# Kernel optimization log

Measured on AMD Instinct MI355X. Metric: run time of the kernel, lower is better.

The kernel has to match this reference:

```python
import jax, jax.numpy as jnp
import numpy as np

B, S, E, H = 32, 4096, 256, 8
P, M = 256, 16  # positions per batch row, tokens per position (pileup depth)


def setup_inputs() -> dict:
    key = jax.random.key(0)
    k1, k2, k3, k4, k5, k6 = jax.random.split(key, 6)
    embeddings = jax.random.normal(k1, (B, S, E), jnp.float32)
    # each position 0..P-1 appears exactly M times per batch row, shuffled
    base = jnp.repeat(jnp.arange(P, dtype=jnp.int32), M)  # (S,)
    positions = jax.vmap(lambda k: jax.random.permutation(k, base))(jax.random.split(k2, B))
    scale = 1.0 / np.sqrt(E)
    Wq = jax.random.normal(k3, (E, E), jnp.float32) * scale
    Wk = jax.random.normal(k4, (E, E), jnp.float32) * scale
    Wv = jax.random.normal(k5, (E, E), jnp.float32) * scale
    W0 = jax.random.normal(k6, (E, E), jnp.float32) * scale
    return {"embeddings": embeddings, "Wq": Wq, "Wk": Wk, "Wv": Wv, "W0": W0,
            "positions": positions, "num_positions": P, "group_size": M, "num_heads": H}


def _intra_group_rank(positions):
    # rank[b,i] = number of earlier tokens j<i in row b with the same position
    Bb, Ss = positions.shape
    idx = jnp.arange(Ss)
    order = jnp.argsort(positions, axis=1)  # stable sort preserves original order within a group
    sp = jnp.take_along_axis(positions, order, axis=1)
    new_group = jnp.concatenate([jnp.ones((Bb, 1), bool), sp[:, 1:] != sp[:, :-1]], axis=1)
    group_start = jax.lax.cummax(jnp.where(new_group, idx[None, :], 0), axis=1)
    rank_sorted = idx[None, :] - group_start
    rank = jnp.zeros_like(positions).at[jnp.arange(Bb)[:, None], order].set(rank_sorted.astype(positions.dtype))
    return rank


def reference(embeddings, Wq, Wk, Wv, W0, positions, num_positions, group_size, num_heads):
    Bb, Ss, Ee = embeddings.shape
    Pp, Mm, Hh = num_positions, group_size, num_heads
    dh = Ee // Hh
    G = Bb * Pp

    valid = positions >= 0
    rank = _intra_group_rank(positions)                       # (B,S) slot within group
    gid = jnp.arange(Bb, dtype=positions.dtype)[:, None] * Pp + jnp.clip(positions, 0)  # (B,S)
    gid_scat = jnp.where(valid, gid, G)                        # out-of-bounds -> dropped

    # gather: ragged regroup into (G, M, E), zero-padded like the torch version
    grouped = jnp.zeros((G, Mm, Ee), embeddings.dtype).at[gid_scat, rank].set(embeddings, mode='drop')

    # multi-head self-attention within each group (no mask, matching the original)
    q = (grouped @ Wq).reshape(G, Mm, Hh, dh)
    k = (grouped @ Wk).reshape(G, Mm, Hh, dh)
    v = (grouped @ Wv).reshape(G, Mm, Hh, dh)
    scores = jnp.einsum('gmhd,gnhd->ghmn', q, k) / np.sqrt(dh).astype(embeddings.dtype)
    attn = jax.nn.softmax(scores, axis=-1)
    ctx = jnp.einsum('ghmn,gnhd->gmhd', attn, v).reshape(G, Mm, Ee)
    att_out = ctx @ W0                                         # (G, M, E)

    # scatter back; invalid (-1) slots stay zero, as in the torch loop
    out = jnp.where(valid[:, :, None], att_out[gid, rank], 0.0)
    return out
```

## Files before the change

kernel.cpp:

```cpp
#include <hip/hip_runtime.h>
#include <stdint.h>

#define B_    32
#define S_    4096
#define E_    256
#define P_    256
#define M_    16
#define G_    (B_*P_)
#define NSLOT (G_*M_)
#define GPW   8
#define ROWS  128
#define NWG   (G_/GPW)

typedef float fv4 __attribute__((ext_vector_type(4)));
typedef int   iv4 __attribute__((ext_vector_type(4)));
typedef int   iv2 __attribute__((ext_vector_type(2)));
typedef __bf16 bv8 __attribute__((ext_vector_type(8)));
typedef short  sv4 __attribute__((ext_vector_type(4)));

__device__ __forceinline__ uint32_t bf16rne(float f) {
  uint32_t u = __builtin_bit_cast(uint32_t, f);
  u += 0x7fffu + ((u >> 16) & 1u);
  return u >> 16;
}
__device__ __forceinline__ uint32_t pk2(uint32_t lo, uint32_t hi) {
  return (lo & 0xffffu) | (hi << 16);
}
__device__ __forceinline__ void mfma32(fv4& d, iv4 a, iv4 b) {
  d = __builtin_amdgcn_mfma_f32_16x16x32_bf16(
        __builtin_bit_cast(bv8, a), __builtin_bit_cast(bv8, b), d, 0, 0, 0);
}
__device__ __forceinline__ void mfma16(fv4& d, iv2 a, iv2 b) {
  d = __builtin_amdgcn_mfma_f32_16x16x16bf16_1k(
        __builtin_bit_cast(sv4, a), __builtin_bit_cast(sv4, b), d, 0, 0, 0);
}
__device__ __forceinline__ void gload_lds16(const void* g, void* l) {
  __builtin_amdgcn_global_load_lds(
      (const __attribute__((address_space(1))) uint32_t*)g,
      (__attribute__((address_space(3))) uint32_t*)l, 16, 0, 0);
}

#define SWZ(off, row) ((off) ^ (((row) & 7) << 4))
#define LQKV(row, cb) ( ((row) >> 1) * 128 + \
    (((((row) & 1) << 6) + (cb)) ^ ((((row) >> 1) & 7) << 4)) )

#define BAR()   { asm volatile("" ::: "memory"); __builtin_amdgcn_s_barrier(); \
                  asm volatile("" ::: "memory"); }
#define VMWAIT1 asm volatile("s_waitcnt vmcnt(1)" ::: "memory")
#define VMWAIT0 asm volatile("s_waitcnt vmcnt(0)" ::: "memory")
#define LGKM0   asm volatile("s_waitcnt lgkmcnt(0)" ::: "memory")

__global__ void k_init(int* cnt, int* s2t) {
  int i = blockIdx.x * 256 + threadIdx.x;
  if (i < G_) cnt[i] = 0;
  if (i < NSLOT) s2t[i] = -1;
}

__global__ void k_trans(const float* __restrict__ Wq, const float* __restrict__ Wk,
                        const float* __restrict__ Wv, const float* __restrict__ W0,
                        uint16_t* __restrict__ WT) {
  int o = blockIdx.x * 256 + threadIdx.x;
  int wsel = blockIdx.y;
  const float* W = (wsel == 0) ? Wq : (wsel == 1) ? Wk : (wsel == 2) ? Wv : W0;
  int n = o >> 8, k = o & 255;
  WT[(size_t)wsel * 65536 + o] = (uint16_t)bf16rne(W[k * 256 + n]);
}

__global__ void k_rank(const int* __restrict__ pos, int* cnt, int* s2t) {
  int i = blockIdx.x * 256 + threadIdx.x;
  if (i >= B_ * S_) return;
  int p = pos[i];
  if (p < 0 || p >= P_) return;
  int b = i >> 12;
  int g = (b << 8) + p;
  int r = atomicAdd(&cnt[g], 1);
  if (r < M_) s2t[g * M_ + r] = i;
}

__device__ __forceinline__ void stage_qkv(const uint16_t* Wt, int c0, char* buf,
                                          int w, int l) {
  int n = w * 2 + (l >> 5);
  int seg = l & 31;
  gload_lds16(reinterpret_cast<const char*>(Wt) + (size_t)(c0 + n) * 512 + SWZ(seg * 16, n),
              buf + w * 1024);
}
__device__ __forceinline__ void stage_w0(const uint16_t* W0T, int c0, char* buf,
                                         int w, int l) {
  int pair = w * 8 + (l >> 3);
  int jp = ((l & 7) * 16) ^ ((pair & 7) << 4);
  int n = 2 * pair + (jp >> 6);
  gload_lds16(reinterpret_cast<const char*>(W0T) + (size_t)n * 512 + c0 * 2 + (jp & 63),
              buf + w * 1024);
}

__global__ __launch_bounds__(1024, 1) void k_main(
    const float* __restrict__ emb, const int* __restrict__ s2t,
    const uint16_t* __restrict__ WT, float* __restrict__ out) {
  extern __shared__ char smem[];
  char* bufA = smem;
  char* bufB = smem + 16384;
  char* Qb = smem + 32768;
  char* Kb = smem + 40960;
  char* Vb = smem + 49152;
  char* Cb = smem + 57344;

  const uint16_t* WqT = WT;
  const uint16_t* WkT = WT + 65536;
  const uint16_t* WvT = WT + 131072;
  const uint16_t* W0T = WT + 196608;

  const int tid = threadIdx.x;
  const int l = tid & 63;
  const int w = tid >> 6;
  const int lane15 = l & 15;
  const int lq = l >> 4;
  const int rb = w >> 1;
  const int ch = w & 1;
  const int slot0 = blockIdx.x * ROWS;

  #pragma unroll 2
  for (int rl = 0; rl < 8; ++rl) {
    int row = w * 8 + rl;
    int t = s2t[slot0 + row];
    uint32_t u0 = 0, u1 = 0;
    if (t >= 0) {
      const float4 v = *reinterpret_cast<const float4*>(emb + (size_t)t * E_ + (l << 2));
      u0 = pk2(bf16rne(v.x), bf16rne(v.y));
      u1 = pk2(bf16rne(v.z), bf16rne(v.w));
    }
    iv2 val; val[0] = (int)u0; val[1] = (int)u1;
    *reinterpret_cast<iv2*>(smem + row * 512 + SWZ(l * 8, row)) = val;
  }
  __syncthreads();

  iv4 xf[8];
  const int arow = rb * 16 + lane15;
  #pragma unroll
  for (int ks = 0; ks < 8; ++ks)
    xf[ks] = *reinterpret_cast<const iv4*>(smem + arow * 512 + SWZ(ks * 64 + lq * 16, arow));
  __syncthreads();

  fv4 outacc[8];
  #pragma unroll
  for (int i = 0; i < 8; ++i) outacc[i] = fv4{0.f, 0.f, 0.f, 0.f};

  stage_qkv(WqT, 0, bufA, w, l);
  stage_qkv(WkT, 0, bufB, w, l);

  for (int hc = 0; hc < 8; ++hc) {
    const int c0 = hc * 32;

    #define COMPUTE_QKV(buf, dst)                                            \
    {                                                                        \
      fv4 a0 = fv4{0.f,0.f,0.f,0.f};                                         \
      const int n0 = ch * 16 + lane15;                                       \
      _Pragma("unroll")                                                      \
      for (int ks = 0; ks < 8; ++ks) {                                       \
        iv4 b0 = *reinterpret_cast<const iv4*>((buf) + n0 * 512 + SWZ(ks * 64 + lq * 16, n0)); \
        mfma32(a0, xf[ks], b0);                                              \
      }                                                                      \
      _Pragma("unroll")                                                      \
      for (int r = 0; r < 4; ++r) {                                          \
        int row = rb * 16 + lq * 4 + r;                                      \
        *reinterpret_cast<uint16_t*>((dst) + LQKV(row, n0 * 2)) =            \
            (uint16_t)bf16rne(a0[r]);                                        \
      }                                                                      \
    }

    VMWAIT1; BAR();
    COMPUTE_QKV(bufA, Qb);
    LGKM0; BAR();
    stage_qkv(WvT, c0, bufA, w, l);

    VMWAIT1; BAR();
    COMPUTE_QKV(bufB, Kb);
    LGKM0; BAR();
    stage_w0(W0T, c0, bufB, w, l);

    VMWAIT1; BAR();
    COMPUTE_QKV(bufA, Vb);
    LGKM0; BAR();
    if (hc < 7) stage_qkv(WqT, c0 + 32, bufA, w, l);

    {
      const int frow = rb * 16 + lane15;
      iv4 kf = *reinterpret_cast<const iv4*>(Kb + LQKV(frow, lq * 16));
      iv4 qf = *reinterpret_cast<const iv4*>(Qb + LQKV(frow, lq * 16));
      fv4 s = fv4{0.f, 0.f, 0.f, 0.f};
      mfma32(s, kf, qf);
      float mx = fmaxf(fmaxf(s[0], s[1]), fmaxf(s[2], s[3]));
      mx = fmaxf(mx, __shfl_xor(mx, 16));
      mx = fmaxf(mx, __shfl_xor(mx, 32));
      const float Cc = 0.25503373f;
      float e0 = exp2f((s[0] - mx) * Cc), e1 = exp2f((s[1] - mx) * Cc);
      float e2 = exp2f((s[2] - mx) * Cc), e3 = exp2f((s[3] - mx) * Cc);
      float sum = e0 + e1 + e2 + e3;
      sum += __shfl_xor(sum, 16);
      sum += __shfl_xor(sum, 32);
      float inv = 1.0f / sum;
      iv2 pa; pa[0] = (int)pk2(bf16rne(e0 * inv), bf16rne(e1 * inv));
              pa[1] = (int)pk2(bf16rne(e2 * inv), bf16rne(e3 * inv));
      const int r0 = rb * 16 + lq * 4;
      const int cb = (ch * 16 + lane15) * 2;
      uint32_t v0 = *reinterpret_cast<const uint16_t*>(Vb + LQKV(r0 + 0, cb));
      uint32_t v1 = *reinterpret_cast<const uint16_t*>(Vb + LQKV(r0 + 1, cb));
      uint32_t v2 = *reinterpret_cast<const uint16_t*>(Vb + LQKV(r0 + 2, cb));
      uint32_t v3 = *reinterpret_cast<const uint16_t*>(Vb + LQKV(r0 + 3, cb));
      iv2 bv; bv[0] = (int)pk2(v0, v1); bv[1] = (int)pk2(v2, v3);
      fv4 cacc = fv4{0.f, 0.f, 0.f, 0.f};
      mfma16(cacc, pa, bv);
      #pragma unroll
      for (int r = 0; r < 4; ++r)
        *reinterpret_cast<uint16_t*>(Cb + LQKV(r0 + r, cb)) =
            (uint16_t)bf16rne(cacc[r]);
    }

    if (hc < 7) { VMWAIT1; } else { VMWAIT0; }
    LGKM0; BAR();
    {
      int ar = rb * 16 + lane15;
      iv4 af = *reinterpret_cast<const iv4*>(Cb + LQKV(ar, lq * 16));
      #pragma unroll
      for (int nt = 0; nt < 8; ++nt) {
        int n = ch * 128 + nt * 16 + lane15;
        iv4 bfg = *reinterpret_cast<const iv4*>(
            bufB + (n >> 1) * 128 + ((((n & 1) << 6) + lq * 16) ^ (((n >> 1) & 7) << 4)));
        mfma32(outacc[nt], af, bfg);
      }
    }
    BAR();
    if (hc < 7) stage_qkv(WkT, c0 + 32, bufB, w, l);
    #undef COMPUTE_QKV
  }

  #pragma unroll
  for (int r = 0; r < 4; ++r) {
    int t = s2t[slot0 + rb * 16 + lq * 4 + r];
    if (t < 0) continue;
    #pragma unroll
    for (int nt = 0; nt < 8; ++nt) {
      int col = ch * 128 + nt * 16 + lane15;
      out[(size_t)t * E_ + col] = outacc[nt][r];
    }
  }
}

extern "C" void kernel_launch(void* const* d_in, const int* in_sizes, int n_in,
                              void* d_out, int out_size, void* d_ws, size_t ws_size,
                              hipStream_t stream) {
  (void)in_sizes; (void)n_in; (void)out_size; (void)ws_size;
  const float* emb = (const float*)d_in[0];
  const float* Wq  = (const float*)d_in[1];
  const float* Wk  = (const float*)d_in[2];
  const float* Wv  = (const float*)d_in[3];
  const float* W0  = (const float*)d_in[4];
  const int*   pos = (const int*)d_in[5];
  float* out = (float*)d_out;

  int* cnt = (int*)d_ws;
  int* s2t = (int*)((char*)d_ws + 32768);
  uint16_t* WT = (uint16_t*)((char*)d_ws + 32768 + 524288);

  (void)hipFuncSetAttribute(reinterpret_cast<const void*>(k_main),
                            hipFuncAttributeMaxDynamicSharedMemorySize, 65536);

  k_init <<<512, 256, 0, stream>>>(cnt, s2t);
  k_trans<<<dim3(256, 4), 256, 0, stream>>>(Wq, Wk, Wv, W0, WT);
  k_rank <<<512, 256, 0, stream>>>(pos, cnt, s2t);
  k_main <<<NWG, 1024, 65536, stream>>>(emb, s2t, WT, out);
}
```

Measured before the change: 177.4 us.

## Use triple-buffered weight staging to prefetch earlier and drop barriers

Replaces the two fixed weight staging buffers with a rotating ring of three 16KB buffers, indexed by a linear stream of 32 weight tiles (Wq, Wk, Wv, W0 per head chunk). Each load is issued right after the barrier, one stage earlier than before, so the load overlaps the current compute and several per-stage barriers go away. LDS grows from 64KB to 80KB, and launch_bounds no longer pins one block per CU. Correctness of buffer reuse now depends on the single barrier per stage plus the vmcnt accounting.

```diff
diff --git a/kernel.cpp b/kernel.cpp
--- a/kernel.cpp
+++ b/kernel.cpp
@@ -46,7 +46,7 @@
 
 #define BAR()   { asm volatile("" ::: "memory"); __builtin_amdgcn_s_barrier(); \
                   asm volatile("" ::: "memory"); }
-#define VMWAIT1 asm volatile("s_waitcnt vmcnt(1)" ::: "memory")
+#define VMWAIT2 asm volatile("s_waitcnt vmcnt(2)" ::: "memory")
 #define VMWAIT0 asm volatile("s_waitcnt vmcnt(0)" ::: "memory")
 #define LGKM0   asm volatile("s_waitcnt lgkmcnt(0)" ::: "memory")
 
@@ -93,21 +93,16 @@
               buf + w * 1024);
 }
 
-__global__ __launch_bounds__(1024, 1) void k_main(
+#undef VMWAIT2
+#define VMWAIT1 asm volatile("s_waitcnt vmcnt(1)" ::: "memory")
+__global__ __launch_bounds__(1024) void k_main(
     const float* __restrict__ emb, const int* __restrict__ s2t,
     const uint16_t* __restrict__ WT, float* __restrict__ out) {
   extern __shared__ char smem[];
-  char* bufA = smem;
-  char* bufB = smem + 16384;
-  char* Qb = smem + 32768;
-  char* Kb = smem + 40960;
-  char* Vb = smem + 49152;
-  char* Cb = smem + 57344;
-
-  const uint16_t* WqT = WT;
-  const uint16_t* WkT = WT + 65536;
-  const uint16_t* WvT = WT + 131072;
-  const uint16_t* W0T = WT + 196608;
+  char* Qb = smem + 49152;
+  char* Kb = smem + 57344;
+  char* Vb = smem + 65536;
+  char* Cb = smem + 73728;
 
   const int tid = threadIdx.x;
   const int l = tid & 63;
@@ -144,11 +139,21 @@
   #pragma unroll
   for (int i = 0; i < 8; ++i) outacc[i] = fv4{0.f, 0.f, 0.f, 0.f};
 
-  stage_qkv(WqT, 0, bufA, w, l);
-  stage_qkv(WkT, 0, bufB, w, l);
+  const uint16_t* W0T = WT + 196608;
+
+  #define ISSUE(j)                                                           \
+    if ((j) < 32) {                                                          \
+      char* bj = smem + ((j) % 3) * 16384;                                   \
+      int kind = (j) & 3, cc = ((j) >> 2) * 32;                              \
+      if (kind == 3) stage_w0(W0T, cc, bj, w, l);                            \
+      else stage_qkv(WT + kind * 65536, cc, bj, w, l);                       \
+    }
+  #define BUF(j) (smem + ((j) % 3) * 16384)
+
+  ISSUE(0); ISSUE(1);
 
   for (int hc = 0; hc < 8; ++hc) {
-    const int c0 = hc * 32;
+    const int t0 = hc * 4;
 
     #define COMPUTE_QKV(buf, dst)                                            \
     {                                                                        \
@@ -168,20 +173,23 @@
     }
 
     VMWAIT1; BAR();
-    COMPUTE_QKV(bufA, Qb);
-    LGKM0; BAR();
-    stage_qkv(WvT, c0, bufA, w, l);
+    ISSUE(t0 + 2);
+    COMPUTE_QKV(BUF(t0), Qb);
+    LGKM0;
 
     VMWAIT1; BAR();
-    COMPUTE_QKV(bufB, Kb);
-    LGKM0; BAR();
-    stage_w0(W0T, c0, bufB, w, l);
+    ISSUE(t0 + 3);
+    COMPUTE_QKV(BUF(t0 + 1), Kb);
+    LGKM0;
 
     VMWAIT1; BAR();
-    COMPUTE_QKV(bufA, Vb);
-    LGKM0; BAR();
-    if (hc < 7) stage_qkv(WqT, c0 + 32, bufA, w, l);
-
+    ISSUE(t0 + 4);
+    COMPUTE_QKV(BUF(t0 + 2), Vb);
+    LGKM0;
+
+    if (t0 + 3 == 31) { VMWAIT0; } else { VMWAIT1; }
+    BAR();
+    ISSUE(t0 + 5);
     {
       const int frow = rb * 16 + lane15;
       iv4 kf = *reinterpret_cast<const iv4*>(Kb + LQKV(frow, lq * 16));
@@ -214,24 +222,25 @@
         *reinterpret_cast<uint16_t*>(Cb + LQKV(r0 + r, cb)) =
             (uint16_t)bf16rne(cacc[r]);
     }
-
-    if (hc < 7) { VMWAIT1; } else { VMWAIT0; }
     LGKM0; BAR();
+
     {
       int ar = rb * 16 + lane15;
       iv4 af = *reinterpret_cast<const iv4*>(Cb + LQKV(ar, lq * 16));
+      char* wb = BUF(t0 + 3);
       #pragma unroll
       for (int nt = 0; nt < 8; ++nt) {
         int n = ch * 128 + nt * 16 + lane15;
         iv4 bfg = *reinterpret_cast<const iv4*>(
-            bufB + (n >> 1) * 128 + ((((n & 1) << 6) + lq * 16) ^ (((n >> 1) & 7) << 4)));
+            wb + (n >> 1) * 128 + ((((n & 1) << 6) + lq * 16) ^ (((n >> 1) & 7) << 4)));
         mfma32(outacc[nt], af, bfg);
       }
     }
-    BAR();
-    if (hc < 7) stage_qkv(WkT, c0 + 32, bufB, w, l);
+    LGKM0;
     #undef COMPUTE_QKV
   }
+  #undef ISSUE
+  #undef BUF
 
   #pragma unroll
   for (int r = 0; r < 4; ++r) {
@@ -262,10 +271,10 @@
   uint16_t* WT = (uint16_t*)((char*)d_ws + 32768 + 524288);
 
   (void)hipFuncSetAttribute(reinterpret_cast<const void*>(k_main),
-                            hipFuncAttributeMaxDynamicSharedMemorySize, 65536);
+                            hipFuncAttributeMaxDynamicSharedMemorySize, 81920);
 
   k_init <<<512, 256, 0, stream>>>(cnt, s2t);
   k_trans<<<dim3(256, 4), 256, 0, stream>>>(Wq, Wk, Wv, W0, WT);
   k_rank <<<512, 256, 0, stream>>>(pos, cnt, s2t);
-  k_main <<<NWG, 1024, 65536, stream>>>(emb, s2t, WT, out);
-}
+  k_main <<<NWG, 1024, 81920, stream>>>(emb, s2t, WT, out);
+}
```

After: 231.2 us. +30.4%, slower.

## Read weight fragments directly from global memory instead of LDS-staged double buffers

Applied to the files above, without the earlier changes.

Removes the asynchronous global-to-LDS double-buffered staging of Wq/Wk/Wv/W0 tiles and instead loads each MFMA B-fragment straight from global memory (the weights are L2-resident bf16). This cuts LDS usage from about 64KB to 32KB, drops the manual vmcnt waits and several barriers, and loosens launch bounds so more than one workgroup might fit per CU. In exchange, weight loads are no longer prefetched or overlapped with compute, so every MFMA step may stall on global or L2 latency, and each wave now fetches weights redundantly.

```diff
diff --git a/kernel.cpp b/kernel.cpp
--- a/kernel.cpp
+++ b/kernel.cpp
@@ -34,21 +34,10 @@
   d = __builtin_amdgcn_mfma_f32_16x16x16bf16_1k(
         __builtin_bit_cast(sv4, a), __builtin_bit_cast(sv4, b), d, 0, 0, 0);
 }
-__device__ __forceinline__ void gload_lds16(const void* g, void* l) {
-  __builtin_amdgcn_global_load_lds(
-      (const __attribute__((address_space(1))) uint32_t*)g,
-      (__attribute__((address_space(3))) uint32_t*)l, 16, 0, 0);
-}
 
 #define SWZ(off, row) ((off) ^ (((row) & 7) << 4))
 #define LQKV(row, cb) ( ((row) >> 1) * 128 + \
     (((((row) & 1) << 6) + (cb)) ^ ((((row) >> 1) & 7) << 4)) )
-
-#define BAR()   { asm volatile("" ::: "memory"); __builtin_amdgcn_s_barrier(); \
-                  asm volatile("" ::: "memory"); }
-#define VMWAIT1 asm volatile("s_waitcnt vmcnt(1)" ::: "memory")
-#define VMWAIT0 asm volatile("s_waitcnt vmcnt(0)" ::: "memory")
-#define LGKM0   asm volatile("s_waitcnt lgkmcnt(0)" ::: "memory")
 
 __global__ void k_init(int* cnt, int* s2t) {
   int i = blockIdx.x * 256 + threadIdx.x;
@@ -77,32 +66,14 @@
   if (r < M_) s2t[g * M_ + r] = i;
 }
 
-__device__ __forceinline__ void stage_qkv(const uint16_t* Wt, int c0, char* buf,
-                                          int w, int l) {
-  int n = w * 2 + (l >> 5);
-  int seg = l & 31;
-  gload_lds16(reinterpret_cast<const char*>(Wt) + (size_t)(c0 + n) * 512 + SWZ(seg * 16, n),
-              buf + w * 1024);
-}
-__device__ __forceinline__ void stage_w0(const uint16_t* W0T, int c0, char* buf,
-                                         int w, int l) {
-  int pair = w * 8 + (l >> 3);
-  int jp = ((l & 7) * 16) ^ ((pair & 7) << 4);
-  int n = 2 * pair + (jp >> 6);
-  gload_lds16(reinterpret_cast<const char*>(W0T) + (size_t)n * 512 + c0 * 2 + (jp & 63),
-              buf + w * 1024);
-}
-
-__global__ __launch_bounds__(1024, 1) void k_main(
+__global__ __launch_bounds__(1024) void k_main(
     const float* __restrict__ emb, const int* __restrict__ s2t,
     const uint16_t* __restrict__ WT, float* __restrict__ out) {
   extern __shared__ char smem[];
-  char* bufA = smem;
-  char* bufB = smem + 16384;
-  char* Qb = smem + 32768;
-  char* Kb = smem + 40960;
-  char* Vb = smem + 49152;
-  char* Cb = smem + 57344;
+  char* Qb = smem;
+  char* Kb = smem + 8192;
+  char* Vb = smem + 16384;
+  char* Cb = smem + 24576;
 
   const uint16_t* WqT = WT;
   const uint16_t* WkT = WT + 65536;
@@ -144,19 +115,18 @@
   #pragma unroll
   for (int i = 0; i < 8; ++i) outacc[i] = fv4{0.f, 0.f, 0.f, 0.f};
 
-  stage_qkv(WqT, 0, bufA, w, l);
-  stage_qkv(WkT, 0, bufB, w, l);
-
   for (int hc = 0; hc < 8; ++hc) {
     const int c0 = hc * 32;
 
-    #define COMPUTE_QKV(buf, dst)                                            \
+    #define PROJ(Wt, dst)                                                    \
     {                                                                        \
       fv4 a0 = fv4{0.f,0.f,0.f,0.f};                                         \
       const int n0 = ch * 16 + lane15;                                       \
+      const char* wb = reinterpret_cast<const char*>(Wt) +                   \
+                       (size_t)(c0 + n0) * 512 + lq * 16;                    \
       _Pragma("unroll")                                                      \
       for (int ks = 0; ks < 8; ++ks) {                                       \
-        iv4 b0 = *reinterpret_cast<const iv4*>((buf) + n0 * 512 + SWZ(ks * 64 + lq * 16, n0)); \
+        iv4 b0 = *reinterpret_cast<const iv4*>(wb + ks * 64);                \
         mfma32(a0, xf[ks], b0);                                              \
       }                                                                      \
       _Pragma("unroll")                                                      \
@@ -166,21 +136,10 @@
             (uint16_t)bf16rne(a0[r]);                                        \
       }                                                                      \
     }
-
-    VMWAIT1; BAR();
-    COMPUTE_QKV(bufA, Qb);
-    LGKM0; BAR();
-    stage_qkv(WvT, c0, bufA, w, l);
-
-    VMWAIT1; BAR();
-    COMPUTE_QKV(bufB, Kb);
-    LGKM0; BAR();
-    stage_w0(W0T, c0, bufB, w, l);
-
-    VMWAIT1; BAR();
-    COMPUTE_QKV(bufA, Vb);
-    LGKM0; BAR();
-    if (hc < 7) stage_qkv(WqT, c0 + 32, bufA, w, l);
+    PROJ(WqT, Qb);
+    PROJ(WkT, Kb);
+    PROJ(WvT, Vb);
+    __syncthreads();
 
     {
       const int frow = rb * 16 + lane15;
@@ -214,9 +173,8 @@
         *reinterpret_cast<uint16_t*>(Cb + LQKV(r0 + r, cb)) =
             (uint16_t)bf16rne(cacc[r]);
     }
-
-    if (hc < 7) { VMWAIT1; } else { VMWAIT0; }
-    LGKM0; BAR();
+    __syncthreads();
+
     {
       int ar = rb * 16 + lane15;
       iv4 af = *reinterpret_cast<const iv4*>(Cb + LQKV(ar, lq * 16));
@@ -224,13 +182,12 @@
       for (int nt = 0; nt < 8; ++nt) {
         int n = ch * 128 + nt * 16 + lane15;
         iv4 bfg = *reinterpret_cast<const iv4*>(
-            bufB + (n >> 1) * 128 + ((((n & 1) << 6) + lq * 16) ^ (((n >> 1) & 7) << 4)));
+            reinterpret_cast<const char*>(W0T) + (size_t)n * 512 + c0 * 2 + lq * 16);
         mfma32(outacc[nt], af, bfg);
       }
     }
-    BAR();
-    if (hc < 7) stage_qkv(WkT, c0 + 32, bufB, w, l);
-    #undef COMPUTE_QKV
+    __syncthreads();
+    #undef PROJ
   }
 
   #pragma unroll
```

Result: slower. 546.2 us (+207.9%).
